# Kernel optimization log

Measured on AMD Instinct MI355X. Metric: run time of the kernel, lower is better.

Reference implementation:

```python
import jax, jax.numpy as jnp
import numpy as np

NUM_TOKENS = 2048
NUM_HEADS = 32
NUM_KV_HEADS = 8
HEAD_DIM = 128
ATTN_SCALE = 0.08838834764831845  # 1/sqrt(head_dim)


def setup_inputs() -> dict:
    key = jax.random.key(0)
    kq, kk, kv = jax.random.split(key, 3)
    q = jax.random.normal(kq, (NUM_TOKENS, NUM_HEADS, HEAD_DIM), dtype=jnp.float32)
    k = jax.random.normal(kk, (NUM_TOKENS, NUM_KV_HEADS, HEAD_DIM), dtype=jnp.float32)
    v = jax.random.normal(kv, (NUM_TOKENS, NUM_KV_HEADS, HEAD_DIM), dtype=jnp.float32)
    return {"q": q, "k": k, "v": v}


def reference(q, k, v):
    # Prefill path: all tokens attend causally; GQA expands kv heads.
    n_rep = NUM_HEADS // NUM_KV_HEADS
    k = jnp.repeat(k, n_rep, axis=1)  # (T, H, D)
    v = jnp.repeat(v, n_rep, axis=1)  # (T, H, D)
    # scores: (H, Tq, Tk)
    scores = jnp.einsum("thd,shd->hts", q, k) * ATTN_SCALE
    T = q.shape[0]
    causal = jnp.tril(jnp.ones((T, T), dtype=bool))  # (Tq, Tk)
    scores = jnp.where(causal[None, :, :], scores, -jnp.inf)
    weights = jax.nn.softmax(scores, axis=-1)
    out = jnp.einsum("hts,shd->thd", weights, v)  # (T, H, D)
    return out
```

## Files before the change

### kernel.cpp

```cpp
#include <hip/hip_runtime.h>

#define NT 2048
#define NH 32
#define NKV 8
#define HD 128
#define BM 128
#define BN 64
#define NQT (NT / BM)
#define SCALE_LOG2E 0.12754984003389239f
#define NEG_BIG -1.0e30f

typedef unsigned int   uint4v  __attribute__((ext_vector_type(4)));
typedef unsigned int   uint2v  __attribute__((ext_vector_type(2)));
typedef float          f32x4   __attribute__((ext_vector_type(4)));
typedef __bf16         bf16x8  __attribute__((ext_vector_type(8)));
typedef unsigned short u16;

#define PK 136
#define PV 72
#define PO 136

__device__ __forceinline__ float bf2f(unsigned u) {
  return __builtin_bit_cast(float, u << 16);
}
__device__ __forceinline__ unsigned f2bf(float f) {
  return (__builtin_bit_cast(unsigned, f) + 0x8000u) >> 16;
}
__device__ __forceinline__ unsigned pack_rn(float lo, float hi) {
  const unsigned ul = __builtin_bit_cast(unsigned, lo) + 0x8000u;
  const unsigned uh = __builtin_bit_cast(unsigned, hi) + 0x8000u;
  return __builtin_amdgcn_perm(ul, uh, 0x03020706u);
}

__global__ __launch_bounds__(256, 2)
void prep_kernel(const float* __restrict__ kg, const float* __restrict__ vg,
                 u16* __restrict__ wsk, u16* __restrict__ wsv) {
  __shared__ __align__(16) float lds_f[32 * 132];
  const int tid = threadIdx.x;
  const int hk  = (int)blockIdx.x >> 6;
  const int kv0 = ((int)blockIdx.x & 63) * 32;

#pragma unroll
  for (int r = 0; r < 4; ++r) {
    const int flat = r * 256 + tid;
    const int row = flat >> 5, q8 = flat & 31;
    const f32x4 a = *(const f32x4*)&kg[((kv0 + row) * NKV + hk) * HD + q8 * 4];
    uint2v pk;
    pk[0] = pack_rn(a[0], a[1]);
    pk[1] = pack_rn(a[2], a[3]);
    *(uint2v*)&wsk[(hk * NT + kv0 + row) * HD + q8 * 4] = pk;
  }
#pragma unroll
  for (int r = 0; r < 4; ++r) {
    const int flat = r * 256 + tid;
    const int row = flat >> 5, q8 = flat & 31;
    *(f32x4*)&lds_f[row * 132 + q8 * 4] =
        *(const f32x4*)&vg[((kv0 + row) * NKV + hk) * HD + q8 * 4];
  }
  __syncthreads();
  const int d = tid >> 1, half = tid & 1;
#pragma unroll
  for (int jj = 0; jj < 2; ++jj) {
    const int j = half * 2 + jj;
    uint4v outw;
#pragma unroll
    for (int e = 0; e < 4; ++e)
      outw[e] = pack_rn(lds_f[(j * 8 + 2 * e) * 132 + d],
                        lds_f[(j * 8 + 2 * e + 1) * 132 + d]);
    *(uint4v*)&wsv[(hk * HD + d) * NT + kv0 + j * 8] = outw;
  }
}

template <bool PRE>
__global__ __launch_bounds__(256, 2)
void fa_kernel(const float* __restrict__ qg, const float* __restrict__ kg,
               const float* __restrict__ vg, float* __restrict__ og,
               const u16* __restrict__ wsk, const u16* __restrict__ wsv) {
  __shared__ __align__(16) u16 lds_k[2][64 * PK];
  __shared__ __align__(16) u16 lds_v[2][HD * PV];

  const int tid  = threadIdx.x;
  const int lane = tid & 63;
  const int w    = tid >> 6;
  const int quad = lane >> 4;
  const int l16  = lane & 15;

  const int h  = blockIdx.x;
  const int hk = h >> 2;
  const int y  = (int)blockIdx.y;
  const int qt = (y < NQT / 2) ? (NQT - 1 - y) : (y - NQT / 2);
  const int q0  = qt * BM;
  const int q0w = q0 + w * 32;

  uint4v qf[2][4];
#pragma unroll
  for (int qn = 0; qn < 2; ++qn)
#pragma unroll
    for (int c = 0; c < 4; ++c) {
      const int row = q0w + qn * 16 + l16;
      const float* qp = &qg[(row * NH + h) * HD + c * 32 + quad * 8];
      const f32x4 a = *(const f32x4*)qp;
      const f32x4 b = *(const f32x4*)(qp + 4);
      uint4v rg;
      rg[0] = pack_rn(a[0] * SCALE_LOG2E, a[1] * SCALE_LOG2E);
      rg[1] = pack_rn(a[2] * SCALE_LOG2E, a[3] * SCALE_LOG2E);
      rg[2] = pack_rn(b[0] * SCALE_LOG2E, b[1] * SCALE_LOG2E);
      rg[3] = pack_rn(b[2] * SCALE_LOG2E, b[3] * SCALE_LOG2E);
      qf[qn][c] = rg;
    }

  f32x4 o[8][2];
#pragma unroll
  for (int nt = 0; nt < 8; ++nt)
#pragma unroll
    for (int qn = 0; qn < 2; ++qn)
#pragma unroll
      for (int r = 0; r < 4; ++r) o[nt][qn][r] = 0.f;

  float l_run[2] = {0.f, 0.f};

  const int njt = 2 * qt + 2;

  uint4v kreg[4], vreg[4];
  f32x4  kregf[4][2], vregf[4][2];

  auto stage_load = [&](int jt) {
    const int kvb = jt * BN;
    if (PRE) {
#pragma unroll
      for (int r = 0; r < 4; ++r) {
        const int flat = r * 256 + tid;
        kreg[r] = *(const uint4v*)&wsk[(hk * NT + kvb + (flat >> 4)) * HD + (flat & 15) * 8];
      }
#pragma unroll
      for (int r = 0; r < 4; ++r) {
        const int flat = r * 256 + tid;
        vreg[r] = *(const uint4v*)&wsv[(hk * HD + (flat >> 3)) * NT + kvb + (flat & 7) * 8];
      }
    } else {
#pragma unroll
      for (int r = 0; r < 4; ++r) {
        const int flat = r * 256 + tid;
        const float* kp = &kg[((kvb + (flat >> 4)) * NKV + hk) * HD + (flat & 15) * 8];
        kregf[r][0] = *(const f32x4*)kp;
        kregf[r][1] = *(const f32x4*)(kp + 4);
      }
#pragma unroll
      for (int r = 0; r < 4; ++r) {
        const int d0 = (r * 4 + w) * 8;
        const float* vp = &vg[((kvb + lane) * NKV + hk) * HD + d0];
        vregf[r][0] = *(const f32x4*)vp;
        vregf[r][1] = *(const f32x4*)(vp + 4);
      }
    }
  };
  auto stage_write = [&](int b) {
    if (PRE) {
#pragma unroll
      for (int r = 0; r < 4; ++r) {
        const int flat = r * 256 + tid;
        *(uint4v*)&lds_k[b][(flat >> 4) * PK + (flat & 15) * 8] = kreg[r];
      }
#pragma unroll
      for (int r = 0; r < 4; ++r) {
        const int flat = r * 256 + tid;
        *(uint4v*)&lds_v[b][(flat >> 3) * PV + (flat & 7) * 8] = vreg[r];
      }
    } else {
#pragma unroll
      for (int r = 0; r < 4; ++r) {
        const int flat = r * 256 + tid;
        uint4v pk;
        pk[0] = pack_rn(kregf[r][0][0], kregf[r][0][1]);
        pk[1] = pack_rn(kregf[r][0][2], kregf[r][0][3]);
        pk[2] = pack_rn(kregf[r][1][0], kregf[r][1][1]);
        pk[3] = pack_rn(kregf[r][1][2], kregf[r][1][3]);
        *(uint4v*)&lds_k[b][(flat >> 4) * PK + (flat & 15) * 8] = pk;
      }
#pragma unroll
      for (int r = 0; r < 4; ++r) {
        const int d0 = (r * 4 + w) * 8;
#pragma unroll
        for (int e = 0; e < 4; ++e) {
          lds_v[b][(d0 + e) * PV + lane]     = (u16)f2bf(vregf[r][0][e]);
          lds_v[b][(d0 + 4 + e) * PV + lane] = (u16)f2bf(vregf[r][1][e]);
        }
      }
    }
  };

  const int sl0 = (quad & 1) * 32 + l16;
  const int sl1 = sl0 + 16;
  const bool qlo = (quad < 2);

  stage_load(0);
  stage_write(0);
  __syncthreads();

  for (int jt = 0; jt < njt; ++jt) {
    const int kv0 = jt * BN;
    const int b   = jt & 1;
    const bool havenext = (jt + 1 < njt);
    if (havenext) stage_load(jt + 1);

    if (kv0 <= q0w + 31) {
      f32x4 s[4][2];
#pragma unroll
      for (int mt = 0; mt < 4; ++mt)
#pragma unroll
        for (int qn = 0; qn < 2; ++qn)
#pragma unroll
          for (int r = 0; r < 4; ++r) s[mt][qn][r] = 0.f;

#pragma unroll
      for (int c = 0; c < 4; ++c) {
#pragma unroll
        for (int mt = 0; mt < 4; ++mt) {
          const uint4v kf = *(uint4v*)&lds_k[b][(mt * 16 + l16) * PK + c * 32 + quad * 8];
#pragma unroll
          for (int qn = 0; qn < 2; ++qn)
            s[mt][qn] = __builtin_amdgcn_mfma_f32_16x16x32_bf16(
                __builtin_bit_cast(bf16x8, kf),
                __builtin_bit_cast(bf16x8, qf[qn][c]), s[mt][qn], 0, 0, 0);
        }
      }

      if (kv0 + BN - 1 > q0w) {
#pragma unroll
        for (int mt = 0; mt < 4; ++mt)
#pragma unroll
          for (int qn = 0; qn < 2; ++qn)
#pragma unroll
            for (int r = 0; r < 4; ++r) {
              const int kvgl = kv0 + mt * 16 + quad * 4 + r;
              const int qgl  = q0w + qn * 16 + l16;
              if (kvgl > qgl) s[mt][qn][r] = NEG_BIG;
            }
      }

      unsigned pk[4][2][2];
#pragma unroll
      for (int qn = 0; qn < 2; ++qn) {
        float ts = 0.f;
#pragma unroll
        for (int mt = 0; mt < 4; ++mt) {
#pragma unroll
          for (int r = 0; r < 4; ++r) {
            const float p = __builtin_amdgcn_exp2f(s[mt][qn][r]);
            s[mt][qn][r] = p;
            ts += p;
          }
          pk[mt][qn][0] = pack_rn(s[mt][qn][0], s[mt][qn][1]);
          pk[mt][qn][1] = pack_rn(s[mt][qn][2], s[mt][qn][3]);
        }
        l_run[qn] += ts;
      }

#pragma unroll
      for (int c2 = 0; c2 < 2; ++c2) {
        uint4v pf[2];
#pragma unroll
        for (int p = 0; p < 4; ++p) {
          const int sl = (p >> 1) ? sl1 : sl0;
#pragma unroll
          for (int qn = 0; qn < 2; ++qn) {
            const int vA = __shfl((int)pk[2 * c2][qn][p & 1], sl);
            const int vB = __shfl((int)pk[2 * c2 + 1][qn][p & 1], sl);
            pf[qn][p] = (unsigned)(qlo ? vA : vB);
          }
        }
#pragma unroll
        for (int nt = 0; nt < 8; ++nt) {
          const uint4v vf = *(uint4v*)&lds_v[b][(nt * 16 + l16) * PV + c2 * 32 + quad * 8];
#pragma unroll
          for (int qn = 0; qn < 2; ++qn)
            o[nt][qn] = __builtin_amdgcn_mfma_f32_16x16x32_bf16(
                __builtin_bit_cast(bf16x8, vf),
                __builtin_bit_cast(bf16x8, pf[qn]), o[nt][qn], 0, 0, 0);
        }
      }
    }

    if (havenext) {
      stage_write((jt + 1) & 1);
      __syncthreads();
    }
  }

  __syncthreads();

  u16* ob = ((u16*)lds_k) + w * 32 * PO;

#pragma unroll
  for (int qn = 0; qn < 2; ++qn) {
    float l = l_run[qn];
    l += __shfl_xor(l, 16);
    l += __shfl_xor(l, 32);
    const float inv = 1.0f / l;
#pragma unroll
    for (int nt = 0; nt < 8; ++nt) {
      uint2v ok2;
      ok2[0] = pack_rn(o[nt][qn][0] * inv, o[nt][qn][1] * inv);
      ok2[1] = pack_rn(o[nt][qn][2] * inv, o[nt][qn][3] * inv);
      *(uint2v*)&ob[(qn * 16 + l16) * PO + nt * 16 + quad * 4] = ok2;
    }
  }
  __asm__ __volatile__("s_waitcnt lgkmcnt(0)" ::: "memory");
#pragma unroll
  for (int rr = 0; rr < 8; ++rr) {
    const int idx = rr * 64 + lane;
    const int row = idx >> 4, ch = idx & 15;
    const uint4v ov = *(uint4v*)&ob[row * PO + ch * 8];
    f32x4 lo, hi;
    lo[0] = bf2f(ov[0] & 0xffffu); lo[1] = bf2f(ov[0] >> 16);
    lo[2] = bf2f(ov[1] & 0xffffu); lo[3] = bf2f(ov[1] >> 16);
    hi[0] = bf2f(ov[2] & 0xffffu); hi[1] = bf2f(ov[2] >> 16);
    hi[2] = bf2f(ov[3] & 0xffffu); hi[3] = bf2f(ov[3] >> 16);
    float* op = &og[((q0 + w * 32 + row) * NH + h) * HD + ch * 8];
    *(f32x4*)op       = lo;
    *(f32x4*)(op + 4) = hi;
  }
}

extern "C" void kernel_launch(void* const* d_in, const int* in_sizes, int n_in,
                              void* d_out, int out_size, void* d_ws, size_t ws_size,
                              hipStream_t stream) {
  (void)in_sizes; (void)n_in; (void)out_size;
  const float* q = (const float*)d_in[0];
  const float* k = (const float*)d_in[1];
  const float* v = (const float*)d_in[2];
  float* out = (float*)d_out;

  const size_t kv_bytes = (size_t)NKV * NT * HD * 2;
  dim3 grid(NH, NQT);
  if (ws_size >= 2 * kv_bytes) {
    u16* wsk = (u16*)d_ws;
    u16* wsv = wsk + (size_t)NKV * NT * HD;
    prep_kernel<<<dim3(NKV * 64), dim3(256), 0, stream>>>(k, v, wsk, wsv);
    fa_kernel<true><<<grid, dim3(256), 0, stream>>>(q, k, v, out, wsk, wsv);
  } else {
    fa_kernel<false><<<grid, dim3(256), 0, stream>>>(q, k, v, out, nullptr, nullptr);
  }
}
```

Measured before the change: 149.8 us.

## Split long causal query tiles across two blocks with combine pass, swizzle LDS

Query tiles 8-15 now split their KV range into two halves handled by separate blocks, each writing unnormalized partial outputs and row sums to workspace, and a new combine kernel merges them. This balances work across the causal triangle and adds blocks. Because the running max is fixed, no max rescaling is needed. The LDS buffers drop from double buffering to a single XOR-swizzled buffer with an extra barrier per iteration, and launch bounds rise to 3 blocks per CU. The epilogue now writes fp32 directly instead of rounding through bf16. The costs are an extra kernel launch, partial-result traffic, and less load/compute overlap.

```diff
diff --git a/kernel.cpp b/kernel.cpp
--- a/kernel.cpp
+++ b/kernel.cpp
@@ -16,13 +16,6 @@
 typedef __bf16         bf16x8  __attribute__((ext_vector_type(8)));
 typedef unsigned short u16;
 
-#define PK 136
-#define PV 72
-#define PO 136
-
-__device__ __forceinline__ float bf2f(unsigned u) {
-  return __builtin_bit_cast(float, u << 16);
-}
 __device__ __forceinline__ unsigned f2bf(float f) {
   return (__builtin_bit_cast(unsigned, f) + 0x8000u) >> 16;
 }
@@ -71,13 +64,15 @@
   }
 }
 
-template <bool PRE>
-__global__ __launch_bounds__(256, 2)
+template <bool PRE, bool SPLIT>
+__global__ __launch_bounds__(256, 3)
 void fa_kernel(const float* __restrict__ qg, const float* __restrict__ kg,
                const float* __restrict__ vg, float* __restrict__ og,
-               const u16* __restrict__ wsk, const u16* __restrict__ wsv) {
-  __shared__ __align__(16) u16 lds_k[2][64 * PK];
-  __shared__ __align__(16) u16 lds_v[2][HD * PV];
+               const u16* __restrict__ wsk, const u16* __restrict__ wsv,
+               float* __restrict__ opart, float* __restrict__ lpart) {
+  __shared__ __align__(16) u16 lds_all[16384];
+  u16* kbuf = lds_all;
+  u16* vbuf = lds_all + 8192;
 
   const int tid  = threadIdx.x;
   const int lane = tid & 63;
@@ -85,10 +80,23 @@
   const int quad = lane >> 4;
   const int l16  = lane & 15;
 
-  const int h  = blockIdx.x;
+  const int h  = blockIdx.y;
   const int hk = h >> 2;
-  const int y  = (int)blockIdx.y;
-  const int qt = (y < NQT / 2) ? (NQT - 1 - y) : (y - NQT / 2);
+
+  int qt, jt0, jt1, ch = 0;
+  bool whole;
+  if (!SPLIT) {
+    qt = (int)gridDim.x - 1 - (int)blockIdx.x;
+    whole = true; jt0 = 0; jt1 = 2 * qt + 2;
+  } else {
+    const int t = (int)blockIdx.x;
+    if (t < 8) { qt = t; whole = true; jt0 = 0; jt1 = 2 * t + 2; }
+    else {
+      const int idx = t - 8;
+      qt = 8 + (idx >> 1); ch = idx & 1; whole = false;
+      jt0 = ch * (qt + 1); jt1 = jt0 + (qt + 1);
+    }
+  }
   const int q0  = qt * BM;
   const int q0w = q0 + w * 32;
 
@@ -119,8 +127,6 @@
 
   float l_run[2] = {0.f, 0.f};
 
-  const int njt = 2 * qt + 2;
-
   uint4v kreg[4], vreg[4];
   f32x4  kregf[4][2], vregf[4][2];
 
@@ -154,36 +160,40 @@
       }
     }
   };
-  auto stage_write = [&](int b) {
+  auto stage_write = [&]() {
     if (PRE) {
 #pragma unroll
       for (int r = 0; r < 4; ++r) {
         const int flat = r * 256 + tid;
-        *(uint4v*)&lds_k[b][(flat >> 4) * PK + (flat & 15) * 8] = kreg[r];
-      }
-#pragma unroll
-      for (int r = 0; r < 4; ++r) {
-        const int flat = r * 256 + tid;
-        *(uint4v*)&lds_v[b][(flat >> 3) * PV + (flat & 7) * 8] = vreg[r];
+        const int row = flat >> 4, c = flat & 15;
+        *(uint4v*)&kbuf[row * 128 + ((c ^ (row & 15)) * 8)] = kreg[r];
+      }
+#pragma unroll
+      for (int r = 0; r < 4; ++r) {
+        const int flat = r * 256 + tid;
+        const int row = flat >> 3, c = flat & 7;
+        *(uint4v*)&vbuf[row * 64 + ((c ^ (row & 7)) * 8)] = vreg[r];
       }
     } else {
 #pragma unroll
       for (int r = 0; r < 4; ++r) {
         const int flat = r * 256 + tid;
+        const int row = flat >> 4, c = flat & 15;
         uint4v pk;
         pk[0] = pack_rn(kregf[r][0][0], kregf[r][0][1]);
         pk[1] = pack_rn(kregf[r][0][2], kregf[r][0][3]);
         pk[2] = pack_rn(kregf[r][1][0], kregf[r][1][1]);
         pk[3] = pack_rn(kregf[r][1][2], kregf[r][1][3]);
-        *(uint4v*)&lds_k[b][(flat >> 4) * PK + (flat & 15) * 8] = pk;
+        *(uint4v*)&kbuf[row * 128 + ((c ^ (row & 15)) * 8)] = pk;
       }
 #pragma unroll
       for (int r = 0; r < 4; ++r) {
         const int d0 = (r * 4 + w) * 8;
 #pragma unroll
-        for (int e = 0; e < 4; ++e) {
-          lds_v[b][(d0 + e) * PV + lane]     = (u16)f2bf(vregf[r][0][e]);
-          lds_v[b][(d0 + 4 + e) * PV + lane] = (u16)f2bf(vregf[r][1][e]);
+        for (int e = 0; e < 8; ++e) {
+          const int d = d0 + e;
+          const float val = (e < 4) ? vregf[r][0][e & 3] : vregf[r][1][e & 3];
+          vbuf[d * 64 + (((lane >> 3) ^ (d & 7)) * 8) + (lane & 7)] = (u16)f2bf(val);
         }
       }
     }
@@ -193,15 +203,14 @@
   const int sl1 = sl0 + 16;
   const bool qlo = (quad < 2);
 
-  stage_load(0);
-  stage_write(0);
+  stage_load(jt0);
+  stage_write();
   __syncthreads();
 
-  for (int jt = 0; jt < njt; ++jt) {
+  for (int jt = jt0; jt < jt1; ++jt) {
     const int kv0 = jt * BN;
-    const int b   = jt & 1;
-    const bool havenext = (jt + 1 < njt);
-    if (havenext) stage_load(jt + 1);
+    const bool more = (jt + 1 < jt1);
+    if (more) stage_load(jt + 1);
 
     if (kv0 <= q0w + 31) {
       f32x4 s[4][2];
@@ -216,7 +225,8 @@
       for (int c = 0; c < 4; ++c) {
 #pragma unroll
         for (int mt = 0; mt < 4; ++mt) {
-          const uint4v kf = *(uint4v*)&lds_k[b][(mt * 16 + l16) * PK + c * 32 + quad * 8];
+          const uint4v kf =
+              *(uint4v*)&kbuf[(mt * 16 + l16) * 128 + (((c * 4 + quad) ^ l16) * 8)];
 #pragma unroll
           for (int qn = 0; qn < 2; ++qn)
             s[mt][qn] = __builtin_amdgcn_mfma_f32_16x16x32_bf16(
@@ -271,7 +281,8 @@
         }
 #pragma unroll
         for (int nt = 0; nt < 8; ++nt) {
-          const uint4v vf = *(uint4v*)&lds_v[b][(nt * 16 + l16) * PV + c2 * 32 + quad * 8];
+          const uint4v vf =
+              *(uint4v*)&vbuf[(nt * 16 + l16) * 64 + (((c2 * 4 + quad) ^ (l16 & 7)) * 8)];
 #pragma unroll
           for (int qn = 0; qn < 2; ++qn)
             o[nt][qn] = __builtin_amdgcn_mfma_f32_16x16x32_bf16(
@@ -281,44 +292,82 @@
       }
     }
 
-    if (havenext) {
-      stage_write((jt + 1) & 1);
+    if (more) {
       __syncthreads();
+      stage_write();
+      __syncthreads();
     }
   }
 
   __syncthreads();
 
-  u16* ob = ((u16*)lds_k) + w * 32 * PO;
-
+  float* fbw = ((float*)lds_all) + w * 2048;
+
+  float inv[2];
 #pragma unroll
   for (int qn = 0; qn < 2; ++qn) {
     float l = l_run[qn];
     l += __shfl_xor(l, 16);
     l += __shfl_xor(l, 32);
-    const float inv = 1.0f / l;
-#pragma unroll
-    for (int nt = 0; nt < 8; ++nt) {
-      uint2v ok2;
-      ok2[0] = pack_rn(o[nt][qn][0] * inv, o[nt][qn][1] * inv);
-      ok2[1] = pack_rn(o[nt][qn][2] * inv, o[nt][qn][3] * inv);
-      *(uint2v*)&ob[(qn * 16 + l16) * PO + nt * 16 + quad * 4] = ok2;
-    }
-  }
-  __asm__ __volatile__("s_waitcnt lgkmcnt(0)" ::: "memory");
-#pragma unroll
-  for (int rr = 0; rr < 8; ++rr) {
-    const int idx = rr * 64 + lane;
-    const int row = idx >> 4, ch = idx & 15;
-    const uint4v ov = *(uint4v*)&ob[row * PO + ch * 8];
-    f32x4 lo, hi;
-    lo[0] = bf2f(ov[0] & 0xffffu); lo[1] = bf2f(ov[0] >> 16);
-    lo[2] = bf2f(ov[1] & 0xffffu); lo[3] = bf2f(ov[1] >> 16);
-    hi[0] = bf2f(ov[2] & 0xffffu); hi[1] = bf2f(ov[2] >> 16);
-    hi[2] = bf2f(ov[3] & 0xffffu); hi[3] = bf2f(ov[3] >> 16);
-    float* op = &og[((q0 + w * 32 + row) * NH + h) * HD + ch * 8];
-    *(f32x4*)op       = lo;
-    *(f32x4*)(op + 4) = hi;
+    inv[qn] = whole ? (1.0f / l) : 1.0f;
+    if (SPLIT && !whole && quad == 0) {
+      lpart[(((h * 8) + (qt - 8)) * 2 + ch) * BM + w * 32 + qn * 16 + l16] = l;
+    }
+  }
+
+  float* obase;
+  int rstride;
+  if (whole) {
+    obase = og + ((size_t)(q0 + w * 32) * NH + h) * HD;
+    rstride = NH * HD;
+  } else {
+    obase = opart + ((((size_t)h * 8) + (qt - 8)) * 2 + ch) * (BM * HD) + (w * 32) * HD;
+    rstride = HD;
+  }
+
+#pragma unroll
+  for (int dh = 0; dh < 2; ++dh) {
+#pragma unroll
+    for (int qn = 0; qn < 2; ++qn) {
+      const int row = qn * 16 + l16;
+#pragma unroll
+      for (int ntl = 0; ntl < 4; ++ntl) {
+        const int nt = dh * 4 + ntl;
+        f32x4 val = o[nt][qn] * inv[qn];
+        const int phys = (ntl * 4 + quad) ^ l16;
+        *(f32x4*)&fbw[row * 64 + phys * 4] = val;
+      }
+    }
+    __asm__ __volatile__("s_waitcnt lgkmcnt(0)" ::: "memory");
+#pragma unroll
+    for (int rr = 0; rr < 8; ++rr) {
+      const int idx = rr * 64 + lane;
+      const int row = idx >> 4, colc = idx & 15;
+      const int phys = colc ^ (row & 15);
+      const f32x4 val = *(f32x4*)&fbw[row * 64 + phys * 4];
+      *(f32x4*)&obase[row * rstride + dh * 64 + colc * 4] = val;
+    }
+    __asm__ __volatile__("s_waitcnt lgkmcnt(0)" ::: "memory");
+  }
+}
+
+__global__ __launch_bounds__(256, 4)
+void combine_kernel(const float* __restrict__ opart, const float* __restrict__ lpart,
+                    float* __restrict__ og) {
+  const int tid = threadIdx.x;
+  const int h   = (int)blockIdx.x & 31;
+  const int q8  = (int)blockIdx.x >> 5;
+  const float* A  = opart + (((size_t)h * 8 + q8) * 2) * (BM * HD);
+  const float* lA = lpart + (((size_t)h * 8 + q8) * 2) * BM;
+#pragma unroll 4
+  for (int i = 0; i < 16; ++i) {
+    const int flat = i * 256 + tid;
+    const int q = flat >> 5, dc = (flat & 31) * 4;
+    const float linv = 1.0f / (lA[q] + lA[BM + q]);
+    const f32x4 a = *(const f32x4*)&A[q * HD + dc];
+    const f32x4 b = *(const f32x4*)&A[BM * HD + q * HD + dc];
+    const f32x4 r = (a + b) * linv;
+    *(f32x4*)&og[((size_t)(1024 + q8 * BM + q) * NH + h) * HD + dc] = r;
   }
 }
 
@@ -331,14 +380,29 @@
   const float* v = (const float*)d_in[2];
   float* out = (float*)d_out;
 
-  const size_t kv_bytes = (size_t)NKV * NT * HD * 2;
-  dim3 grid(NH, NQT);
-  if (ws_size >= 2 * kv_bytes) {
+  const size_t kv_elts  = (size_t)NKV * NT * HD;
+  const size_t kv_bytes = kv_elts * 2;
+  const size_t op_flt   = (size_t)NH * 8 * 2 * BM * HD;
+  const size_t lp_flt   = (size_t)NH * 8 * 2 * BM;
+  const size_t need_split = 2 * kv_bytes + (op_flt + lp_flt) * 4;
+
+  if (ws_size >= need_split) {
     u16* wsk = (u16*)d_ws;
-    u16* wsv = wsk + (size_t)NKV * NT * HD;
+    u16* wsv = wsk + kv_elts;
+    float* opart = (float*)(wsv + kv_elts);
+    float* lpart = opart + op_flt;
     prep_kernel<<<dim3(NKV * 64), dim3(256), 0, stream>>>(k, v, wsk, wsv);
-    fa_kernel<true><<<grid, dim3(256), 0, stream>>>(q, k, v, out, wsk, wsv);
+    fa_kernel<true, true><<<dim3(24, NH), dim3(256), 0, stream>>>(
+        q, k, v, out, wsk, wsv, opart, lpart);
+    combine_kernel<<<dim3(NH * 8), dim3(256), 0, stream>>>(opart, lpart, out);
+  } else if (ws_size >= 2 * kv_bytes) {
+    u16* wsk = (u16*)d_ws;
+    u16* wsv = wsk + kv_elts;
+    prep_kernel<<<dim3(NKV * 64), dim3(256), 0, stream>>>(k, v, wsk, wsv);
+    fa_kernel<true, false><<<dim3(NQT, NH), dim3(256), 0, stream>>>(
+        q, k, v, out, wsk, wsv, nullptr, nullptr);
   } else {
-    fa_kernel<false><<<grid, dim3(256), 0, stream>>>(q, k, v, out, nullptr, nullptr);
-  }
-}
+    fa_kernel<false, false><<<dim3(NQT, NH), dim3(256), 0, stream>>>(
+        q, k, v, out, nullptr, nullptr, nullptr, nullptr);
+  }
+}
```

Measured after the change: 236.4 us. 57.8% more time.
